# Optimization experiments

Hardware: AMD Instinct MI355X
Metric: run time of the kernel (lower is better)

The kernel has to match this reference:

```python
import jax, jax.numpy as jnp
import numpy as np

EPS = 1e-5  # InstanceNorm2d default eps


def setup_inputs() -> dict:
    key = jax.random.key(0)
    ks = jax.random.split(key, 5)
    B, T, C, N, H = 4, 8, 256, 196, 4
    s = 1.0 / np.sqrt(C)
    return {
        "emb": jax.random.normal(ks[0], (B, T, C, N), dtype=jnp.float32),
        "Wq": jax.random.normal(ks[1], (H, C, C), dtype=jnp.float32) * s,
        "Wk": jax.random.normal(ks[2], (H, C, C), dtype=jnp.float32) * s,
        "Wv": jax.random.normal(ks[3], (H, C, C), dtype=jnp.float32) * s,
        "Wo": jax.random.normal(ks[4], (C, C), dtype=jnp.float32) * s,
    }


def reference(emb, Wq, Wk, Wv, Wo):
    B, T, C, N = emb.shape
    S = T * N  # KV_size
    # emb.permute(0,1,3,2).view(B, T*N, C)
    x = jnp.transpose(emb, (0, 1, 3, 2)).reshape(B, S, C)
    # per-head full-width Linear projections (nn.Linear: y = x @ W.T)
    Q = jnp.einsum("bsc,hdc->bhsd", x, Wq)  # [B,H,S,C]
    K = jnp.einsum("bsc,hdc->bhsd", x, Wk)
    V = jnp.einsum("bsc,hdc->bhsd", x, Wv)
    scores = jnp.einsum("bhsd,bhtd->bhst", Q, K) / jnp.sqrt(jnp.float32(S))
    # InstanceNorm2d over each [S,S] map per (batch, head), no affine, biased var
    mean = jnp.mean(scores, axis=(-2, -1), keepdims=True)
    var = jnp.var(scores, axis=(-2, -1), keepdims=True)
    normed = (scores - mean) * jax.lax.rsqrt(var + EPS)
    probs = jax.nn.softmax(normed, axis=-1)  # attn_dropout: eval-mode identity
    ctx = jnp.einsum("bhst,bhtd->bhsd", probs, V)  # [B,H,S,C]
    ctx = jnp.mean(ctx, axis=1)  # mean over heads -> [B,S,C]
    O1 = jnp.einsum("bsc,dc->bsd", ctx, Wo)  # out Linear; proj_dropout identity
    # .view(-1, num_frames, num_channels, num_patches) on contiguous [B, T*N, C]
    return O1.reshape(B, T, C, N)
```

## Files before the change

### kernel.cpp

```cpp
#include <hip/hip_runtime.h>
#include <stdint.h>

typedef unsigned short u16;

#define Bb 4
#define Hh 4
#define Tt 8
#define Cc 256
#define NP 196
#define Ss 1568
#define SCALE_S 0.0252538136f
#define LST 32

typedef __attribute__((ext_vector_type(4))) float floatx4;
typedef __attribute__((ext_vector_type(8))) short shortx8;

__device__ __forceinline__ float bf2f(u16 u) {
    union { unsigned u; float f; } v; v.u = ((unsigned)u) << 16; return v.f;
}
__device__ __forceinline__ u16 f2bf(float f) {
    union { float f; unsigned u; } v; v.f = f;
    unsigned r = v.u + 0x7FFFu + ((v.u >> 16) & 1u);
    return (u16)(r >> 16);
}

__global__ __launch_bounds__(256) void k_convall(const float* __restrict__ Wq,
                                                 const float* __restrict__ Wk,
                                                 const float* __restrict__ Wv,
                                                 const float* __restrict__ Wo,
                                                 u16* __restrict__ dst) {
    const int NW = Hh * Cc * Cc;
    int i = blockIdx.x * 256 + threadIdx.x;
    float v;
    if (i < NW) v = Wq[i];
    else if (i < 2 * NW) v = Wk[i - NW];
    else if (i < 3 * NW) v = Wv[i - 2 * NW];
    else if (i < 3 * NW + Cc * Cc) v = Wo[i - 3 * NW];
    else return;
    dst[i] = f2bf(v);
}

__device__ __forceinline__ void mfma_step(const u16* As, const u16* Bs, int lane,
                                          int wm, int wn, floatx4 acc[4][4]) {
    const int r15 = lane & 15;
    const int kq  = (lane >> 4) << 3;
    shortx8 a[4], b[4];
#pragma unroll
    for (int i = 0; i < 4; ++i)
        a[i] = *(const shortx8*)(As + (wm * 64 + i * 16 + r15) * LST + kq);
#pragma unroll
    for (int j = 0; j < 4; ++j)
        b[j] = *(const shortx8*)(Bs + (wn * 64 + j * 16 + r15) * LST + kq);
#pragma unroll
    for (int i = 0; i < 4; ++i)
#pragma unroll
        for (int j = 0; j < 4; ++j)
            acc[i][j] = __builtin_amdgcn_mfma_f32_16x16x32_bf16(a[i], b[j], acc[i][j], 0, 0, 0);
}

__device__ __forceinline__ void gemm_bt_core(const u16* A, const u16* Bm, int lda, int ldb,
                                             int mbase, int mlast, int nbase, int nlast,
                                             int KD, u16* As, u16* Bs, floatx4 acc[4][4]) {
    int tid = threadIdx.x;
    int lane = tid & 63, wave = tid >> 6, wm = wave >> 1, wn = wave & 1;
    int row0 = tid >> 2, row1 = 64 + row0;
    int cole = (tid & 3) << 3;
    int ga0 = mbase + row0; ga0 = ga0 <= mlast ? ga0 : mlast;
    int ga1 = mbase + row1; ga1 = ga1 <= mlast ? ga1 : mlast;
    int gb0 = nbase + row0; gb0 = gb0 <= nlast ? gb0 : nlast;
    int gb1 = nbase + row1; gb1 = gb1 <= nlast ? gb1 : nlast;
    const u16* pa0 = A  + (size_t)ga0 * lda + cole;
    const u16* pa1 = A  + (size_t)ga1 * lda + cole;
    const u16* pb0 = Bm + (size_t)gb0 * ldb + cole;
    const u16* pb1 = Bm + (size_t)gb1 * ldb + cole;
    shortx8 xa0 = *(const shortx8*)(pa0),      xa1 = *(const shortx8*)(pa1);
    shortx8 xb0 = *(const shortx8*)(pb0),      xb1 = *(const shortx8*)(pb1);
    shortx8 ya0 = *(const shortx8*)(pa0 + 32), ya1 = *(const shortx8*)(pa1 + 32);
    shortx8 yb0 = *(const shortx8*)(pb0 + 32), yb1 = *(const shortx8*)(pb1 + 32);
    for (int k0 = 0; k0 < KD; k0 += 64) {
        __syncthreads();
        *(shortx8*)(As + row0 * LST + cole) = xa0;
        *(shortx8*)(As + row1 * LST + cole) = xa1;
        *(shortx8*)(Bs + row0 * LST + cole) = xb0;
        *(shortx8*)(Bs + row1 * LST + cole) = xb1;
        int kp = k0 + 64;
        if (kp < KD) {
            xa0 = *(const shortx8*)(pa0 + kp); xa1 = *(const shortx8*)(pa1 + kp);
            xb0 = *(const shortx8*)(pb0 + kp); xb1 = *(const shortx8*)(pb1 + kp);
        }
        __syncthreads();
        mfma_step(As, Bs, lane, wm, wn, acc);
        if (k0 + 32 < KD) {
            __syncthreads();
            *(shortx8*)(As + row0 * LST + cole) = ya0;
            *(shortx8*)(As + row1 * LST + cole) = ya1;
            *(shortx8*)(Bs + row0 * LST + cole) = yb0;
            *(shortx8*)(Bs + row1 * LST + cole) = yb1;
            int kq2 = k0 + 96;
            if (kq2 < KD) {
                ya0 = *(const shortx8*)(pa0 + kq2); ya1 = *(const shortx8*)(pa1 + kq2);
                yb0 = *(const shortx8*)(pb0 + kq2); yb1 = *(const shortx8*)(pb1 + kq2);
            }
            __syncthreads();
            mfma_step(As, Bs, lane, wm, wn, acc);
        }
    }
}

__global__ void k_transpose(const float* __restrict__ emb, u16* __restrict__ x) {
    __shared__ u16 tile[32][33];
    int bt = blockIdx.z;
    int c0 = blockIdx.y * 32, n0 = blockIdx.x * 32;
    const float* src = emb + (size_t)bt * Cc * NP;
#pragma unroll
    for (int rr = 0; rr < 32; rr += 8) {
        int c = c0 + threadIdx.y + rr;
        int n = n0 + threadIdx.x;
        u16 v = 0;
        if (n < NP) v = f2bf(src[(size_t)c * NP + n]);
        tile[threadIdx.y + rr][threadIdx.x] = v;
    }
    __syncthreads();
    int b = bt / Tt, t = bt % Tt;
    u16* dst = x + ((size_t)b * Ss + (size_t)t * NP) * Cc;
#pragma unroll
    for (int rr = 0; rr < 32; rr += 8) {
        int n = n0 + threadIdx.y + rr;
        int c = c0 + threadIdx.x;
        if (n < NP) dst[(size_t)n * Cc + c] = tile[threadIdx.x][threadIdx.y + rr];
    }
}

__global__ __launch_bounds__(256) void k_qkv(const u16* __restrict__ x,
                                             const u16* __restrict__ Wall,
                                             u16* __restrict__ Q, u16* __restrict__ Kb,
                                             u16* __restrict__ Vt) {
    __shared__ __align__(16) u16 As[128 * LST], Bs[128 * LST];
    floatx4 acc[4][4];
#pragma unroll
    for (int i = 0; i < 4; ++i)
#pragma unroll
        for (int j = 0; j < 4; ++j) acc[i][j] = (floatx4)(0.f);
    int z = blockIdx.z;
    int qkv = z >> 4, bh = z & 15, b = bh >> 2, h = bh & 3;
    const u16* A = x + (size_t)b * Ss * Cc;
    const u16* W = Wall + (size_t)qkv * Hh * Cc * Cc + (size_t)h * Cc * Cc;
    int mbase = blockIdx.y * 128, nbase = blockIdx.x * 128;
    gemm_bt_core(A, W, Cc, Cc, mbase, Ss - 1, nbase, Cc - 1, Cc, As, Bs, acc);

    int tid = threadIdx.x, lane = tid & 63, wave = tid >> 6, wm = wave >> 1, wn = wave & 1;
    int rq = (lane >> 4) << 2, cn = lane & 15;
    if (qkv < 2) {
        u16* out = (qkv == 0 ? Q : Kb) + (size_t)bh * Ss * Cc;
#pragma unroll
        for (int i = 0; i < 4; ++i) {
            int mb = mbase + wm * 64 + i * 16 + rq;
#pragma unroll
            for (int j = 0; j < 4; ++j) {
                int n = nbase + wn * 64 + j * 16 + cn;
#pragma unroll
                for (int r = 0; r < 4; ++r) {
                    int m = mb + r;
                    if (m < Ss) out[(size_t)m * Cc + n] = f2bf(acc[i][j][r]);
                }
            }
        }
    } else {
        u16* out = Vt + (size_t)bh * Cc * Ss;
#pragma unroll
        for (int i = 0; i < 4; ++i) {
            int m0 = mbase + wm * 64 + i * 16 + rq;
            if (m0 < Ss) {
#pragma unroll
                for (int j = 0; j < 4; ++j) {
                    int n = nbase + wn * 64 + j * 16 + cn;
                    ushort4 v;
                    v.x = f2bf(acc[i][j][0]); v.y = f2bf(acc[i][j][1]);
                    v.z = f2bf(acc[i][j][2]); v.w = f2bf(acc[i][j][3]);
                    *(ushort4*)(out + (size_t)n * Ss + m0) = v;
                }
            }
        }
    }
}

__global__ __launch_bounds__(256) void k_scores(const u16* __restrict__ Q,
                                                const u16* __restrict__ Kb,
                                                u16* __restrict__ Sc, float* __restrict__ stats) {
    __shared__ __align__(16) u16 As[128 * LST], Bs[128 * LST];
    __shared__ float sred[8];
    floatx4 acc[4][4];
#pragma unroll
    for (int i = 0; i < 4; ++i)
#pragma unroll
        for (int j = 0; j < 4; ++j) acc[i][j] = (floatx4)(0.f);
    int bh = blockIdx.z;
    const u16* A  = Q  + (size_t)bh * Ss * Cc;
    const u16* Bm = Kb + (size_t)bh * Ss * Cc;
    int mbase = blockIdx.y * 128, nbase = blockIdx.x * 128;
    gemm_bt_core(A, Bm, Cc, Cc, mbase, Ss - 1, nbase, Ss - 1, Cc, As, Bs, acc);

    int tid = threadIdx.x, lane = tid & 63, wave = tid >> 6, wm = wave >> 1, wn = wave & 1;
    int rq = (lane >> 4) << 2, cn = lane & 15;
    u16* out = Sc + (size_t)bh * Ss * Ss;
    float lsum = 0.f, lsq = 0.f;
#pragma unroll
    for (int i = 0; i < 4; ++i) {
        int mb = mbase + wm * 64 + i * 16 + rq;
#pragma unroll
        for (int j = 0; j < 4; ++j) {
            int n = nbase + wn * 64 + j * 16 + cn;
            bool nv = n < Ss;
#pragma unroll
            for (int r = 0; r < 4; ++r) {
                int m = mb + r;
                if (nv && m < Ss) {
                    float v = acc[i][j][r] * SCALE_S;
                    out[(size_t)m * Ss + n] = f2bf(v);
                    lsum += v; lsq += v * v;
                }
            }
        }
    }
#pragma unroll
    for (int mk = 1; mk <= 32; mk <<= 1) { lsum += __shfl_xor(lsum, mk); lsq += __shfl_xor(lsq, mk); }
    if (lane == 0) { sred[wave] = lsum; sred[4 + wave] = lsq; }
    __syncthreads();
    if (tid == 0) atomicAdd(&stats[bh * 4 + 0], sred[0] + sred[1] + sred[2] + sred[3]);
    if (tid == 1) atomicAdd(&stats[bh * 4 + 1], sred[4] + sred[5] + sred[6] + sred[7]);
}

__global__ __launch_bounds__(256) void k_pv(const u16* __restrict__ Sc,
                                            const u16* __restrict__ Vt,
                                            const float* __restrict__ stats,
                                            float* __restrict__ ctxm) {
    __shared__ __align__(16) u16 As[64 * LST], Bs[128 * LST];
    __shared__ float rs[64];
    floatx4 acc[2][4];
#pragma unroll
    for (int i = 0; i < 2; ++i)
#pragma unroll
        for (int j = 0; j < 4; ++j) acc[i][j] = (floatx4)(0.f);
    int bh = blockIdx.z;
    float inv  = 1.f / ((float)Ss * (float)Ss);
    float mean = stats[bh * 4] * inv;
    float var  = fmaxf(stats[bh * 4 + 1] * inv - mean * mean, 0.f);
    float istd = rsqrtf(var + 1e-5f);
    float aa = istd * 1.44269504f;
    float bb = -mean * aa;
    const u16* A  = Sc + (size_t)bh * Ss * Ss;
    const u16* Bm = Vt + (size_t)bh * Cc * Ss;
    int mbase = blockIdx.y * 64;
    int nbase = blockIdx.x * 128;
    int tid = threadIdx.x, lane = tid & 63, wave = tid >> 6;
    int wr = wave >> 1, wc = wave & 1;
    int rowA = tid >> 2;
    int cole = (tid & 3) << 3;
    int ga = mbase + rowA; ga = ga <= Ss - 1 ? ga : Ss - 1;
    const u16* pa  = A + (size_t)ga * Ss + cole;
    const u16* pb0 = Bm + (size_t)(nbase + rowA) * Ss + cole;
    const u16* pb1 = Bm + (size_t)(nbase + 64 + rowA) * Ss + cole;
    float rsum = 0.f;

    auto ldexp8 = [&](const u16* p) -> shortx8 {
        shortx8 v = *(const shortx8*)(p);
        shortx8 o;
        float s = 0.f;
#pragma unroll
        for (int e = 0; e < 8; ++e) {
            float ex = exp2f(bf2f((u16)v[e]) * aa + bb);
            s += ex; o[e] = (short)f2bf(ex);
        }
        rsum += s;
        return o;
    };

    const int r15 = lane & 15;
    const int kq  = (lane >> 4) << 3;

    shortx8 xa = ldexp8(pa),        ya = ldexp8(pa + 32);
    shortx8 xb0 = *(const shortx8*)(pb0),      xb1 = *(const shortx8*)(pb1);
    shortx8 yb0 = *(const shortx8*)(pb0 + 32), yb1 = *(const shortx8*)(pb1 + 32);

    for (int k0 = 0; k0 < Ss; k0 += 64) {
        __syncthreads();
        *(shortx8*)(As + rowA * LST + cole) = xa;
        *(shortx8*)(Bs + rowA * LST + cole) = xb0;
        *(shortx8*)(Bs + (64 + rowA) * LST + cole) = xb1;
        int kp = k0 + 64;
        if (kp < Ss) {
            xa  = ldexp8(pa + kp);
            xb0 = *(const shortx8*)(pb0 + kp);
            xb1 = *(const shortx8*)(pb1 + kp);
        }
        __syncthreads();
        {
            shortx8 a[2], b[4];
#pragma unroll
            for (int i = 0; i < 2; ++i)
                a[i] = *(const shortx8*)(As + (wr * 32 + i * 16 + r15) * LST + kq);
#pragma unroll
            for (int j = 0; j < 4; ++j)
                b[j] = *(const shortx8*)(Bs + (wc * 64 + j * 16 + r15) * LST + kq);
#pragma unroll
            for (int i = 0; i < 2; ++i)
#pragma unroll
                for (int j = 0; j < 4; ++j)
                    acc[i][j] = __builtin_amdgcn_mfma_f32_16x16x32_bf16(a[i], b[j], acc[i][j], 0, 0, 0);
        }
        if (k0 + 32 < Ss) {
            __syncthreads();
            *(shortx8*)(As + rowA * LST + cole) = ya;
            *(shortx8*)(Bs + rowA * LST + cole) = yb0;
            *(shortx8*)(Bs + (64 + rowA) * LST + cole) = yb1;
            int kq2 = k0 + 96;
            if (kq2 < Ss) {
                ya  = ldexp8(pa + kq2);
                yb0 = *(const shortx8*)(pb0 + kq2);
                yb1 = *(const shortx8*)(pb1 + kq2);
            }
            __syncthreads();
            shortx8 a[2], b[4];
#pragma unroll
            for (int i = 0; i < 2; ++i)
                a[i] = *(const shortx8*)(As + (wr * 32 + i * 16 + r15) * LST + kq);
#pragma unroll
            for (int j = 0; j < 4; ++j)
                b[j] = *(const shortx8*)(Bs + (wc * 64 + j * 16 + r15) * LST + kq);
#pragma unroll
            for (int i = 0; i < 2; ++i)
#pragma unroll
                for (int j = 0; j < 4; ++j)
                    acc[i][j] = __builtin_amdgcn_mfma_f32_16x16x32_bf16(a[i], b[j], acc[i][j], 0, 0, 0);
        }
    }
    rsum += __shfl_xor(rsum, 1); rsum += __shfl_xor(rsum, 2);
    __syncthreads();
    if ((tid & 3) == 0) rs[rowA] = rsum;
    __syncthreads();

    int b = bh >> 2;
    float* outp = ctxm + (size_t)b * Ss * Cc;
    int rq = (lane >> 4) << 2, cn = lane & 15;
#pragma unroll
    for (int i = 0; i < 2; ++i) {
        int ml = wr * 32 + i * 16 + rq;
#pragma unroll
        for (int r = 0; r < 4; ++r) {
            int m = mbase + ml + r;
            if (m < Ss) {
                float invs = 0.25f / rs[ml + r];
#pragma unroll
                for (int j = 0; j < 4; ++j) {
                    int n = nbase + wc * 64 + j * 16 + cn;
                    atomicAdd(&outp[(size_t)m * Cc + n], acc[i][j][r] * invs);
                }
            }
        }
    }
}

__global__ __launch_bounds__(256) void k_out(const float* __restrict__ ctxm,
                                             const u16* __restrict__ Wo, float* __restrict__ out) {
    __shared__ __align__(16) u16 As[128 * LST], Bs[128 * LST];
    floatx4 acc[4][4];
#pragma unroll
    for (int i = 0; i < 4; ++i)
#pragma unroll
        for (int j = 0; j < 4; ++j) acc[i][j] = (floatx4)(0.f);
    int b = blockIdx.z;
    const float* A = ctxm + (size_t)b * Ss * Cc;
    int mbase = blockIdx.y * 128, nbase = blockIdx.x * 128;
    int tid = threadIdx.x, lane = tid & 63, wave = tid >> 6, wm = wave >> 1, wn = wave & 1;
    int row0 = tid >> 2, row1 = 64 + row0;
    int cole = (tid & 3) << 3;
    int ga0 = mbase + row0; ga0 = ga0 <= Ss - 1 ? ga0 : Ss - 1;
    int ga1 = mbase + row1; ga1 = ga1 <= Ss - 1 ? ga1 : Ss - 1;
    const float* pa0 = A + (size_t)ga0 * Cc + cole;
    const float* pa1 = A + (size_t)ga1 * Cc + cole;
    const u16* pb0 = Wo + (size_t)(nbase + row0 <= Cc - 1 ? nbase + row0 : Cc - 1) * Cc + cole;
    const u16* pb1 = Wo + (size_t)(nbase + row1 <= Cc - 1 ? nbase + row1 : Cc - 1) * Cc + cole;
    float4 a00 = *(const float4*)(pa0), a01 = *(const float4*)(pa0 + 4);
    float4 a10 = *(const float4*)(pa1), a11 = *(const float4*)(pa1 + 4);
    shortx8 vb0 = *(const shortx8*)(pb0);
    shortx8 vb1 = *(const shortx8*)(pb1);
    for (int k0 = 0; k0 < Cc; k0 += 32) {
        shortx8 o0, o1;
        o0[0] = (short)f2bf(a00.x); o0[1] = (short)f2bf(a00.y); o0[2] = (short)f2bf(a00.z); o0[3] = (short)f2bf(a00.w);
        o0[4] = (short)f2bf(a01.x); o0[5] = (short)f2bf(a01.y); o0[6] = (short)f2bf(a01.z); o0[7] = (short)f2bf(a01.w);
        o1[0] = (short)f2bf(a10.x); o1[1] = (short)f2bf(a10.y); o1[2] = (short)f2bf(a10.z); o1[3] = (short)f2bf(a10.w);
        o1[4] = (short)f2bf(a11.x); o1[5] = (short)f2bf(a11.y); o1[6] = (short)f2bf(a11.z); o1[7] = (short)f2bf(a11.w);
        __syncthreads();
        *(shortx8*)(As + row0 * LST + cole) = o0;
        *(shortx8*)(As + row1 * LST + cole) = o1;
        *(shortx8*)(Bs + row0 * LST + cole) = vb0;
        *(shortx8*)(Bs + row1 * LST + cole) = vb1;
        int k1 = k0 + 32;
        if (k1 < Cc) {
            a00 = *(const float4*)(pa0 + k1); a01 = *(const float4*)(pa0 + k1 + 4);
            a10 = *(const float4*)(pa1 + k1); a11 = *(const float4*)(pa1 + k1 + 4);
            vb0 = *(const shortx8*)(pb0 + k1);
            vb1 = *(const shortx8*)(pb1 + k1);
        }
        __syncthreads();
        mfma_step(As, Bs, lane, wm, wn, acc);
    }
    int rq = (lane >> 4) << 2, cn = lane & 15;
    float* o = out + (size_t)b * Ss * Cc;
#pragma unroll
    for (int i = 0; i < 4; ++i) {
        int mb = mbase + wm * 64 + i * 16 + rq;
#pragma unroll
        for (int j = 0; j < 4; ++j) {
            int n = nbase + wn * 64 + j * 16 + cn;
#pragma unroll
            for (int r = 0; r < 4; ++r) {
                int m = mb + r;
                if (m < Ss) o[(size_t)m * Cc + n] = acc[i][j][r];
            }
        }
    }
}

extern "C" void kernel_launch(void* const* d_in, const int* in_sizes, int n_in,
                              void* d_out, int out_size, void* d_ws, size_t ws_size,
                              hipStream_t stream) {
    const float* emb = (const float*)d_in[0];
    float* out = (float*)d_out;

    char* ws = (char*)d_ws;
    size_t off = 0;
    auto alloc = [&](size_t bytes) -> void* {
        void* p = ws + off;
        off = (off + bytes + 255) & ~(size_t)255;
        return p;
    };
    float* stats = (float*)alloc(16 * 4 * sizeof(float));
    u16* Wall = (u16*)alloc((size_t)(3 * Hh + 1) * Cc * Cc * 2);
    u16* x    = (u16*)alloc((size_t)Bb * Ss * Cc * 2);
    u16* Q    = (u16*)alloc((size_t)Bb * Hh * Ss * Cc * 2);
    u16* Kb   = (u16*)alloc((size_t)Bb * Hh * Ss * Cc * 2);
    u16* Vt   = (u16*)alloc((size_t)Bb * Hh * Ss * Cc * 2);
    float* ctxm = (float*)alloc((size_t)Bb * Ss * Cc * 4);
    u16* Sc   = (u16*)alloc((size_t)Bb * Hh * Ss * Ss * 2);
    u16* Woc  = Wall + (size_t)3 * Hh * Cc * Cc;

    hipMemsetAsync(stats, 0, 16 * 4 * sizeof(float), stream);
    hipMemsetAsync(ctxm, 0, (size_t)Bb * Ss * Cc * 4, stream);

    k_convall<<<dim3(3328), dim3(256), 0, stream>>>((const float*)d_in[1], (const float*)d_in[2],
                                                    (const float*)d_in[3], (const float*)d_in[4], Wall);
    k_transpose<<<dim3(7, 8, 32), dim3(32, 8), 0, stream>>>(emb, x);
    k_qkv<<<dim3(2, 13, 48), dim3(256), 0, stream>>>(x, Wall, Q, Kb, Vt);
    k_scores<<<dim3(13, 13, 16), dim3(256), 0, stream>>>(Q, Kb, Sc, stats);
    k_pv<<<dim3(2, 25, 16), dim3(256), 0, stream>>>(Sc, Vt, stats, ctxm);
    k_out<<<dim3(2, 13, 4), dim3(256), 0, stream>>>(ctxm, Woc, out);
}
```

Measured before the change: 243.6 us.

## Fuse scores recompute with softmax and PV, drop materialized score matrix

The bf16 score matrix is no longer written to global memory. The stats pass now only accumulates sum and sum-of-squares. A new fused kernel recomputes QK^T per 32-row tile, applies the normalized exp, stages P in LDS and multiplies by V directly. Both launches are flattened with an XCD-aware block mapping so each (batch, head) stays on one XCD for cache locality. This removes roughly 80 MB of score writes and reads, at the cost of computing QK^T twice and reading K and V straight from global memory without LDS tiling.

New measurement: 346.3 us. 1.42x slower.

```diff
diff --git a/kernel.cpp b/kernel.cpp
--- a/kernel.cpp
+++ b/kernel.cpp
@@ -11,6 +11,8 @@
 #define Ss 1568
 #define SCALE_S 0.0252538136f
 #define LST 32
+#define LQ 264
+#define LP 136
 
 typedef __attribute__((ext_vector_type(4))) float floatx4;
 typedef __attribute__((ext_vector_type(8))) short shortx8;
@@ -184,9 +186,9 @@
     }
 }
 
-__global__ __launch_bounds__(256) void k_scores(const u16* __restrict__ Q,
-                                                const u16* __restrict__ Kb,
-                                                u16* __restrict__ Sc, float* __restrict__ stats) {
+__global__ __launch_bounds__(256) void k_stats(const u16* __restrict__ Q,
+                                               const u16* __restrict__ Kb,
+                                               float* __restrict__ stats) {
     __shared__ __align__(16) u16 As[128 * LST], Bs[128 * LST];
     __shared__ float sred[8];
     floatx4 acc[4][4];
@@ -194,15 +196,17 @@
     for (int i = 0; i < 4; ++i)
 #pragma unroll
         for (int j = 0; j < 4; ++j) acc[i][j] = (floatx4)(0.f);
-    int bh = blockIdx.z;
+    int L = blockIdx.x;
+    int xcd = L & 7, idx = L >> 3;
+    int bh = xcd + 8 * (idx / 169);
+    int rem = idx % 169;
+    int mbase = (rem / 13) * 128, nbase = (rem % 13) * 128;
     const u16* A  = Q  + (size_t)bh * Ss * Cc;
     const u16* Bm = Kb + (size_t)bh * Ss * Cc;
-    int mbase = blockIdx.y * 128, nbase = blockIdx.x * 128;
     gemm_bt_core(A, Bm, Cc, Cc, mbase, Ss - 1, nbase, Ss - 1, Cc, As, Bs, acc);
 
     int tid = threadIdx.x, lane = tid & 63, wave = tid >> 6, wm = wave >> 1, wn = wave & 1;
     int rq = (lane >> 4) << 2, cn = lane & 15;
-    u16* out = Sc + (size_t)bh * Ss * Ss;
     float lsum = 0.f, lsq = 0.f;
 #pragma unroll
     for (int i = 0; i < 4; ++i) {
@@ -216,7 +220,6 @@
                 int m = mb + r;
                 if (nv && m < Ss) {
                     float v = acc[i][j][r] * SCALE_S;
-                    out[(size_t)m * Ss + n] = f2bf(v);
                     lsum += v; lsq += v * v;
                 }
             }
@@ -230,131 +233,151 @@
     if (tid == 1) atomicAdd(&stats[bh * 4 + 1], sred[4] + sred[5] + sred[6] + sred[7]);
 }
 
-__global__ __launch_bounds__(256) void k_pv(const u16* __restrict__ Sc,
-                                            const u16* __restrict__ Vt,
-                                            const float* __restrict__ stats,
-                                            float* __restrict__ ctxm) {
-    __shared__ __align__(16) u16 As[64 * LST], Bs[128 * LST];
-    __shared__ float rs[64];
-    floatx4 acc[2][4];
-#pragma unroll
-    for (int i = 0; i < 2; ++i)
-#pragma unroll
-        for (int j = 0; j < 4; ++j) acc[i][j] = (floatx4)(0.f);
-    int bh = blockIdx.z;
+__global__ __launch_bounds__(256) void k_fused(const u16* __restrict__ Q,
+                                               const u16* __restrict__ Kb,
+                                               const u16* __restrict__ Vt,
+                                               const float* __restrict__ stats,
+                                               float* __restrict__ ctxm) {
+    __shared__ __align__(16) u16 Qs[32 * LQ];
+    __shared__ __align__(16) u16 Ps[32 * LP];
+    __shared__ float rsw[4][32];
+    __shared__ float rs2[32];
+
+    int L = blockIdx.x;
+    int xcd = L & 7, idx = L >> 3;
+    int bh = xcd + 8 * (idx / 49);
+    int mt = idx % 49;
+    int mbase = mt * 32;
+
     float inv  = 1.f / ((float)Ss * (float)Ss);
     float mean = stats[bh * 4] * inv;
     float var  = fmaxf(stats[bh * 4 + 1] * inv - mean * mean, 0.f);
     float istd = rsqrtf(var + 1e-5f);
-    float aa = istd * 1.44269504f;
-    float bb = -mean * aa;
-    const u16* A  = Sc + (size_t)bh * Ss * Ss;
-    const u16* Bm = Vt + (size_t)bh * Cc * Ss;
-    int mbase = blockIdx.y * 64;
-    int nbase = blockIdx.x * 128;
+    float aa   = istd * 1.44269504f;
+    float aas  = aa * SCALE_S;
+    float bb   = -mean * aa;
+
+    const u16* Qp = Q  + (size_t)bh * Ss * Cc;
+    const u16* Kp = Kb + (size_t)bh * Ss * Cc;
+    const u16* Vp = Vt + (size_t)bh * Cc * Ss;
+
     int tid = threadIdx.x, lane = tid & 63, wave = tid >> 6;
-    int wr = wave >> 1, wc = wave & 1;
-    int rowA = tid >> 2;
-    int cole = (tid & 3) << 3;
-    int ga = mbase + rowA; ga = ga <= Ss - 1 ? ga : Ss - 1;
-    const u16* pa  = A + (size_t)ga * Ss + cole;
-    const u16* pb0 = Bm + (size_t)(nbase + rowA) * Ss + cole;
-    const u16* pb1 = Bm + (size_t)(nbase + 64 + rowA) * Ss + cole;
-    float rsum = 0.f;
-
-    auto ldexp8 = [&](const u16* p) -> shortx8 {
-        shortx8 v = *(const shortx8*)(p);
-        shortx8 o;
-        float s = 0.f;
-#pragma unroll
-        for (int e = 0; e < 8; ++e) {
-            float ex = exp2f(bf2f((u16)v[e]) * aa + bb);
-            s += ex; o[e] = (short)f2bf(ex);
-        }
-        rsum += s;
-        return o;
-    };
-
     const int r15 = lane & 15;
     const int kq  = (lane >> 4) << 3;
-
-    shortx8 xa = ldexp8(pa),        ya = ldexp8(pa + 32);
-    shortx8 xb0 = *(const shortx8*)(pb0),      xb1 = *(const shortx8*)(pb1);
-    shortx8 yb0 = *(const shortx8*)(pb0 + 32), yb1 = *(const shortx8*)(pb1 + 32);
-
-    for (int k0 = 0; k0 < Ss; k0 += 64) {
-        __syncthreads();
-        *(shortx8*)(As + rowA * LST + cole) = xa;
-        *(shortx8*)(Bs + rowA * LST + cole) = xb0;
-        *(shortx8*)(Bs + (64 + rowA) * LST + cole) = xb1;
-        int kp = k0 + 64;
-        if (kp < Ss) {
-            xa  = ldexp8(pa + kp);
-            xb0 = *(const shortx8*)(pb0 + kp);
-            xb1 = *(const shortx8*)(pb1 + kp);
-        }
-        __syncthreads();
+    const int prow = (lane >> 4) << 2;
+
+    {
+        int r = tid >> 3, c0 = (tid & 7) << 3;
+        const u16* src = Qp + (size_t)(mbase + r) * Cc + c0;
+#pragma unroll
+        for (int p = 0; p < 4; ++p)
+            *(shortx8*)(Qs + r * LQ + c0 + p * 64) = *(const shortx8*)(src + p * 64);
+    }
+    __syncthreads();
+
+    floatx4 accc[2][4];
+#pragma unroll
+    for (int i = 0; i < 2; ++i)
+#pragma unroll
+        for (int j = 0; j < 4; ++j) accc[i][j] = (floatx4)(0.f);
+    floatx4 rsf[2];
+    rsf[0] = (floatx4)(0.f); rsf[1] = (floatx4)(0.f);
+
+    for (int kc = 0; kc < Ss; kc += 128) {
+        floatx4 accs[2][2];
+        accs[0][0] = (floatx4)(0.f); accs[0][1] = (floatx4)(0.f);
+        accs[1][0] = (floatx4)(0.f); accs[1][1] = (floatx4)(0.f);
+        const u16* kb0; const u16* kb1;
         {
-            shortx8 a[2], b[4];
+            int kr0 = kc + wave * 32 + r15;
+            int kr1 = kr0 + 16;
+            kb0 = Kp + (size_t)(kr0 < Ss ? kr0 : 0) * Cc + kq;
+            kb1 = Kp + (size_t)(kr1 < Ss ? kr1 : 0) * Cc + kq;
+        }
+#pragma unroll
+        for (int t = 0; t < 8; ++t) {
+            shortx8 a0 = *(const shortx8*)(Qs + r15 * LQ + t * 32 + kq);
+            shortx8 a1 = *(const shortx8*)(Qs + (16 + r15) * LQ + t * 32 + kq);
+            shortx8 b0 = *(const shortx8*)(kb0 + t * 32);
+            shortx8 b1 = *(const shortx8*)(kb1 + t * 32);
+            accs[0][0] = __builtin_amdgcn_mfma_f32_16x16x32_bf16(a0, b0, accs[0][0], 0, 0, 0);
+            accs[1][0] = __builtin_amdgcn_mfma_f32_16x16x32_bf16(a1, b0, accs[1][0], 0, 0, 0);
+            accs[0][1] = __builtin_amdgcn_mfma_f32_16x16x32_bf16(a0, b1, accs[0][1], 0, 0, 0);
+            accs[1][1] = __builtin_amdgcn_mfma_f32_16x16x32_bf16(a1, b1, accs[1][1], 0, 0, 0);
+        }
+        float exv[2][2][4];
+#pragma unroll
+        for (int jn = 0; jn < 2; ++jn) {
+            bool valid = (kc + wave * 32 + jn * 16 + r15) < Ss;
 #pragma unroll
             for (int i = 0; i < 2; ++i)
-                a[i] = *(const shortx8*)(As + (wr * 32 + i * 16 + r15) * LST + kq);
-#pragma unroll
-            for (int j = 0; j < 4; ++j)
-                b[j] = *(const shortx8*)(Bs + (wc * 64 + j * 16 + r15) * LST + kq);
+#pragma unroll
+                for (int r = 0; r < 4; ++r) {
+                    float ex = valid ? exp2f(accs[i][jn][r] * aas + bb) : 0.f;
+                    exv[jn][i][r] = ex;
+                    rsf[i][r] += ex;
+                }
+        }
+        __syncthreads();
+#pragma unroll
+        for (int jn = 0; jn < 2; ++jn) {
+            int pcol = wave * 32 + jn * 16 + r15;
 #pragma unroll
             for (int i = 0; i < 2; ++i)
 #pragma unroll
-                for (int j = 0; j < 4; ++j)
-                    acc[i][j] = __builtin_amdgcn_mfma_f32_16x16x32_bf16(a[i], b[j], acc[i][j], 0, 0, 0);
-        }
-        if (k0 + 32 < Ss) {
-            __syncthreads();
-            *(shortx8*)(As + rowA * LST + cole) = ya;
-            *(shortx8*)(Bs + rowA * LST + cole) = yb0;
-            *(shortx8*)(Bs + (64 + rowA) * LST + cole) = yb1;
-            int kq2 = k0 + 96;
-            if (kq2 < Ss) {
-                ya  = ldexp8(pa + kq2);
-                yb0 = *(const shortx8*)(pb0 + kq2);
-                yb1 = *(const shortx8*)(pb1 + kq2);
-            }
-            __syncthreads();
-            shortx8 a[2], b[4];
-#pragma unroll
-            for (int i = 0; i < 2; ++i)
-                a[i] = *(const shortx8*)(As + (wr * 32 + i * 16 + r15) * LST + kq);
-#pragma unroll
-            for (int j = 0; j < 4; ++j)
-                b[j] = *(const shortx8*)(Bs + (wc * 64 + j * 16 + r15) * LST + kq);
-#pragma unroll
-            for (int i = 0; i < 2; ++i)
-#pragma unroll
-                for (int j = 0; j < 4; ++j)
-                    acc[i][j] = __builtin_amdgcn_mfma_f32_16x16x32_bf16(a[i], b[j], acc[i][j], 0, 0, 0);
-        }
-    }
-    rsum += __shfl_xor(rsum, 1); rsum += __shfl_xor(rsum, 2);
+                for (int r = 0; r < 4; ++r)
+                    Ps[(prow + r + 16 * i) * LP + pcol] = f2bf(exv[jn][i][r]);
+        }
+        __syncthreads();
+#pragma unroll
+        for (int t = 0; t < 4; ++t) {
+            int vcol = kc + t * 32 + kq;
+            const u16* vb = Vp + (vcol + 8 <= Ss ? vcol : 0);
+            shortx8 a0 = *(const shortx8*)(Ps + r15 * LP + t * 32 + kq);
+            shortx8 a1 = *(const shortx8*)(Ps + (16 + r15) * LP + t * 32 + kq);
+#pragma unroll
+            for (int j = 0; j < 4; ++j) {
+                int vrow = wave * 64 + j * 16 + r15;
+                shortx8 bV = *(const shortx8*)(vb + (size_t)vrow * Ss);
+                accc[0][j] = __builtin_amdgcn_mfma_f32_16x16x32_bf16(a0, bV, accc[0][j], 0, 0, 0);
+                accc[1][j] = __builtin_amdgcn_mfma_f32_16x16x32_bf16(a1, bV, accc[1][j], 0, 0, 0);
+            }
+        }
+    }
+
+#pragma unroll
+    for (int i = 0; i < 2; ++i)
+#pragma unroll
+        for (int r = 0; r < 4; ++r) {
+            float v = rsf[i][r];
+            v += __shfl_xor(v, 1); v += __shfl_xor(v, 2);
+            v += __shfl_xor(v, 4); v += __shfl_xor(v, 8);
+            rsf[i][r] = v;
+        }
+    if (r15 == 0) {
+#pragma unroll
+        for (int i = 0; i < 2; ++i)
+#pragma unroll
+            for (int r = 0; r < 4; ++r)
+                rsw[wave][prow + r + 16 * i] = rsf[i][r];
+    }
     __syncthreads();
-    if ((tid & 3) == 0) rs[rowA] = rsum;
+    if (tid < 32) rs2[tid] = rsw[0][tid] + rsw[1][tid] + rsw[2][tid] + rsw[3][tid];
     __syncthreads();
 
     int b = bh >> 2;
     float* outp = ctxm + (size_t)b * Ss * Cc;
-    int rq = (lane >> 4) << 2, cn = lane & 15;
 #pragma unroll
     for (int i = 0; i < 2; ++i) {
-        int ml = wr * 32 + i * 16 + rq;
 #pragma unroll
         for (int r = 0; r < 4; ++r) {
-            int m = mbase + ml + r;
-            if (m < Ss) {
-                float invs = 0.25f / rs[ml + r];
-#pragma unroll
-                for (int j = 0; j < 4; ++j) {
-                    int n = nbase + wc * 64 + j * 16 + cn;
-                    atomicAdd(&outp[(size_t)m * Cc + n], acc[i][j][r] * invs);
-                }
+            int ml = prow + r + 16 * i;
+            float invs = 0.25f / rs2[ml];
+            int m = mbase + ml;
+#pragma unroll
+            for (int j = 0; j < 4; ++j) {
+                int n = wave * 64 + j * 16 + r15;
+                atomicAdd(&outp[(size_t)m * Cc + n], accc[i][j][r] * invs);
             }
         }
     }
@@ -442,7 +465,6 @@
     u16* Kb   = (u16*)alloc((size_t)Bb * Hh * Ss * Cc * 2);
     u16* Vt   = (u16*)alloc((size_t)Bb * Hh * Ss * Cc * 2);
     float* ctxm = (float*)alloc((size_t)Bb * Ss * Cc * 4);
-    u16* Sc   = (u16*)alloc((size_t)Bb * Hh * Ss * Ss * 2);
     u16* Woc  = Wall + (size_t)3 * Hh * Cc * Cc;
 
     hipMemsetAsync(stats, 0, 16 * 4 * sizeof(float), stream);
@@ -452,7 +474,7 @@
                                                     (const float*)d_in[3], (const float*)d_in[4], Wall);
     k_transpose<<<dim3(7, 8, 32), dim3(32, 8), 0, stream>>>(emb, x);
     k_qkv<<<dim3(2, 13, 48), dim3(256), 0, stream>>>(x, Wall, Q, Kb, Vt);
-    k_scores<<<dim3(13, 13, 16), dim3(256), 0, stream>>>(Q, Kb, Sc, stats);
-    k_pv<<<dim3(2, 25, 16), dim3(256), 0, stream>>>(Sc, Vt, stats, ctxm);
+    k_stats<<<dim3(2704), dim3(256), 0, stream>>>(Q, Kb, stats);
+    k_fused<<<dim3(784), dim3(256), 0, stream>>>(Q, Kb, Vt, stats, ctxm);
     k_out<<<dim3(2, 13, 4), dim3(256), 0, stream>>>(ctxm, Woc, out);
 }
```
